# Performance work log

Hardware: AMD Instinct MI355X
Metric: run time of the kernel (lower is better)

The kernel has to match this reference:

```python
import jax, jax.numpy as jnp
import numpy as np

N = 100000      # nodes
E = 1600000     # edges
D_IN = 128
D_H = 128
D_OUT = 32
NUM_LAYERS = 3


def setup_inputs() -> dict:
    key = jax.random.key(0)
    ks = jax.random.split(key, 12)
    x = jax.random.normal(ks[0], (N, D_IN), dtype=jnp.float32)
    edge_index = jax.random.randint(ks[1], (2, E), 0, N, dtype=jnp.int64)
    def lin(k, fan_in, fan_out):
        bound = 1.0 / np.sqrt(fan_in)
        kw, kb = jax.random.split(k)
        W = jax.random.uniform(kw, (fan_in, fan_out), jnp.float32, -bound, bound)
        b = jax.random.uniform(kb, (fan_out,), jnp.float32, -bound, bound)
        return W, b
    W0, b0 = lin(ks[2], D_IN, D_H)
    W1, b1 = lin(ks[3], D_H, D_H)
    W2, b2 = lin(ks[4], D_H, D_H)
    Wfc, bfc = lin(ks[5], D_H, D_OUT)
    return {"x": x, "edge_index": edge_index, "W0": W0, "b0": b0,
            "W1": W1, "b1": b1, "W2": W2, "b2": b2, "Wfc": Wfc, "bfc": bfc}


def reference(x, edge_index, W0, b0, W1, b1, W2, b2, Wfc, bfc):
    n = x.shape[0]
    # add self-loops once (PyG GCNConv default add_self_loops=True)
    loop = jnp.arange(n, dtype=edge_index.dtype)
    src = jnp.concatenate([edge_index[0], loop])  # [E+N]
    dst = jnp.concatenate([edge_index[1], loop])
    # symmetric degree normalization: deg computed over destination (col)
    deg = jax.ops.segment_sum(jnp.ones_like(dst, dtype=x.dtype), dst, num_segments=n)
    dis = jnp.where(deg > 0, jax.lax.rsqrt(deg), 0.0)  # deg^{-1/2}, inf->0
    norm = (dis[src] * dis[dst])[:, None]              # [E+N, 1]

    def gcn_conv(h, W, b):
        h = h @ W                                       # [N, d_out]
        agg = jax.ops.segment_sum(h[src] * norm, dst, num_segments=n)
        return agg + b                                  # bias after aggregation

    h = x
    for (W, b) in ((W0, b0), (W1, b1), (W2, b2)):
        h = jax.nn.relu(gcn_conv(h, W, b))              # dropout p=0 -> identity
    pooled = jnp.mean(h, axis=0)                        # [D_H]
    return pooled @ Wfc + bfc                           # [D_OUT]
```

## Files before the change

### kernel.cpp

```cpp
#include <hip/hip_runtime.h>
#include <hip/hip_bf16.h>
#include <cstdint>


typedef unsigned short u16;
typedef unsigned int u32;
typedef unsigned char u8;
typedef __attribute__((ext_vector_type(8))) short short8v;
typedef __attribute__((ext_vector_type(4))) float f32x4;
typedef __attribute__((ext_vector_type(2))) float f32x2;

#define NBMAX 256
#define BKSH  9
#define SCH   2048
#define CAP   12288

__device__ inline u16 f2bf(float f) {
  u32 u = __float_as_uint(f);
  u += 0x7fff + ((u >> 16) & 1);
  return (u16)(u >> 16);
}
__device__ inline float bflo(u32 u) { return __uint_as_float(u << 16); }
__device__ inline float bfhi(u32 u) { return __uint_as_float(u & 0xffff0000u); }

__global__ void k_init(const int* __restrict__ ei, int* __restrict__ mode,
                       int* __restrict__ bucketCur, float* __restrict__ pooled,
                       int e, int nb) {
  if (blockIdx.x == 0) {
    __shared__ int any;
    if (threadIdx.x == 0) any = 0;
    __syncthreads();
    int lim = min(e, 2048);
    int local = 0;
    for (int i = threadIdx.x; i < lim; i += blockDim.x)
      local |= (ei[2 * i + 1] != 0);
    if (local) atomicOr(&any, 1);
    __syncthreads();
    if (threadIdx.x == 0) mode[0] = (any == 0) ? 1 : 0;
  } else {
    int i = threadIdx.x;
    if (i < nb) bucketCur[i] = 0;
    if (i < 128) pooled[i] = 0.0f;
  }
}

__global__ __launch_bounds__(256) void b_scatter(const int* __restrict__ ei,
                                                 const int* __restrict__ mode,
                                                 int* __restrict__ bucketCur,
                                                 int* __restrict__ pairBuf,
                                                 int e, int nb) {
  __shared__ int cnt[NBMAX];
  __shared__ int pre[NBMAX];
  __shared__ int base[NBMAX];
  __shared__ int stage[2 * SCH];
  const int t = threadIdx.x;
  const int chunk0 = blockIdx.x * SCH;
  const int nloc = min(SCH, e - chunk0);
  const int m = mode[0];

  cnt[t] = 0;
  __syncthreads();

  int myS[SCH / 256], myD[SCH / 256], myB[SCH / 256], mySlot[SCH / 256];
#pragma unroll
  for (int j = 0; j < SCH / 256; ++j) {
    int li = j * 256 + t;
    myB[j] = -1;
    if (li < nloc) {
      int i = chunk0 + li;
      long long di = (long long)e + i;
      int s = m ? ei[2 * (long long)i] : ei[i];
      int d = m ? ei[2 * di] : ei[di];
      int b = d >> BKSH;
      myS[j] = s; myD[j] = d; myB[j] = b;
      mySlot[j] = atomicAdd(&cnt[b], 1);
    }
  }
  __syncthreads();

  int c0 = cnt[t];
  pre[t] = c0;
  __syncthreads();
  for (int d = 1; d < NBMAX; d <<= 1) {
    int v = (t >= d) ? pre[t - d] : 0;
    __syncthreads();
    pre[t] += v;
    __syncthreads();
  }
  int myPre = pre[t] - c0;
  if (t < nb && c0 > 0) base[t] = atomicAdd(&bucketCur[t], c0);
  __syncthreads();
  cnt[t] = myPre;
  __syncthreads();

#pragma unroll
  for (int j = 0; j < SCH / 256; ++j) {
    if (myB[j] >= 0) {
      int si = cnt[myB[j]] + mySlot[j];
      stage[2 * si] = myS[j];
      stage[2 * si + 1] = myD[j];
    }
  }
  __syncthreads();

  int wave = t >> 6, lane = t & 63;
  for (int b = wave; b < nb; b += 4) {
    int cb = pre[b] - cnt[b];
    if (cb <= 0) continue;
    int lo = cnt[b];
    int gb = base[b];
    int room = CAP - gb;
    int allowed = (room > 0) ? min(cb, room) : 0;
    size_t dst = ((size_t)b * CAP + gb) * 2;
    for (int j = lane; j < 2 * allowed; j += 64)
      pairBuf[dst + j] = stage[2 * lo + j];
  }
}

__global__ __launch_bounds__(256) void b_bscan2(const int* __restrict__ bucketCur,
                                                int* __restrict__ bucketOff, int nb) {
  __shared__ int sh[NBMAX];
  int t = threadIdx.x;
  int c = (t < nb) ? bucketCur[t] : 0;
  sh[t] = c;
  __syncthreads();
  for (int d = 1; d < NBMAX; d <<= 1) {
    int v = (t >= d) ? sh[t - d] : 0;
    __syncthreads();
    sh[t] += v;
    __syncthreads();
  }
  if (t < nb) bucketOff[t] = sh[t] - c;
}

__global__ __launch_bounds__(512) void b_fine(const int* __restrict__ pairBuf,
                                              const int* __restrict__ bucketCur,
                                              const int* __restrict__ bucketOff,
                                              int* __restrict__ offs,
                                              float* __restrict__ dis,
                                              int* __restrict__ csr,
                                              int n, int e) {
  const int b = blockIdx.x;
  const int d0 = b << BKSH;
  const size_t pb = (size_t)b * CAP;
  const int cnt = bucketCur[b];
  const int lo = bucketOff[b];
  __shared__ int arr[1 << BKSH];
  __shared__ int cur[1 << BKSH];
  const int t = threadIdx.x;
  arr[t] = 0; cur[t] = 0;
  __syncthreads();
  for (int i = t; i < cnt; i += 512) {
    int d = pairBuf[2 * (pb + i) + 1];
    atomicAdd(&arr[d - d0], 1);
  }
  __syncthreads();
  int c0 = arr[t];
  __syncthreads();
  for (int dd = 1; dd < 512; dd <<= 1) {
    int v = (t >= dd) ? arr[t - dd] : 0;
    __syncthreads();
    arr[t] += v;
    __syncthreads();
  }
  int epre = arr[t] - c0;
  int gd = d0 + t;
  if (gd < n) {
    offs[gd] = lo + epre;
    dis[gd] = rsqrtf((float)c0 + 1.0f);
  }
  __syncthreads();
  arr[t] = epre;
  __syncthreads();
  for (int i = t; i < cnt; i += 512) {
    int s = pairBuf[2 * (pb + i)];
    int d = pairBuf[2 * (pb + i) + 1];
    int ld = d - d0;
    int p = lo + arr[ld] + atomicAdd(&cur[ld], 1);
    csr[p] = s;
  }
  if (b == 0 && t == 0) offs[n] = e;
}

__global__ __launch_bounds__(256) void k_wpack3(const float* __restrict__ W0,
                                                const float* __restrict__ W1,
                                                const float* __restrict__ W2,
                                                u16* __restrict__ wp) {
  int f = blockIdx.x * 256 + threadIdx.x;
  int wsel = f >> 11;
  int li = f & 2047;
  const float* W = (wsel == 0) ? W0 : (wsel == 1) ? W1 : W2;
  u16* dst = wp + (size_t)wsel * 2048 * 8;
  int ct = li >> 8, kc = (li >> 6) & 3, lane = li & 63;
  int g = lane >> 4, c = lane & 15;
  u32 o[4];
#pragma unroll
  for (int q = 0; q < 4; ++q) {
    int k = kc * 32 + g * 8 + q * 2;
    u16 e0 = f2bf(W[(size_t)k * 128 + ct * 16 + c]);
    u16 e1 = f2bf(W[(size_t)(k + 1) * 128 + ct * 16 + c]);
    o[q] = (u32)e0 | ((u32)e1 << 16);
  }
  uint4 v; v.x = o[0]; v.y = o[1]; v.z = o[2]; v.w = o[3];
  *reinterpret_cast<uint4*>(dst + (size_t)li * 8) = v;
}

template <bool FP32IN>
__global__ __launch_bounds__(256) void k_gemm_mfma(const void* __restrict__ hin,
                                                   const u16* __restrict__ wp,
                                                   const float* __restrict__ dis,
                                                   u8* __restrict__ tmpf8, int n) {
  __shared__ float eps[64 * 132];
  const int tid = threadIdx.x;
  const int w = tid >> 6, l = tid & 63;
  const int g = l >> 4, c16 = l & 15;
  const int rowbase = blockIdx.x * 64 + w * 16;

  const short8v zero8 = {0, 0, 0, 0, 0, 0, 0, 0};
  short8v a[4];
  int ar = rowbase + c16;
  bool aok = ar < n;
#pragma unroll
  for (int kc = 0; kc < 4; ++kc) {
    if (FP32IN) {
      const float* hrow = (const float*)hin + (size_t)ar * 128;
      short8v s = zero8;
      if (aok) {
        float4 v0 = *reinterpret_cast<const float4*>(hrow + kc * 32 + g * 8);
        float4 v1 = *reinterpret_cast<const float4*>(hrow + kc * 32 + g * 8 + 4);
        s[0] = (short)f2bf(v0.x); s[1] = (short)f2bf(v0.y);
        s[2] = (short)f2bf(v0.z); s[3] = (short)f2bf(v0.w);
        s[4] = (short)f2bf(v1.x); s[5] = (short)f2bf(v1.y);
        s[6] = (short)f2bf(v1.z); s[7] = (short)f2bf(v1.w);
      }
      a[kc] = s;
    } else {
      const u16* hrow = (const u16*)hin + (size_t)ar * 128;
      a[kc] = aok ? *reinterpret_cast<const short8v*>(hrow + kc * 32 + g * 8) : zero8;
    }
  }

  f32x4 acc[8];
#pragma unroll
  for (int ct = 0; ct < 8; ++ct) acc[ct] = f32x4{0.f, 0.f, 0.f, 0.f};

#pragma unroll
  for (int ct = 0; ct < 8; ++ct) {
#pragma unroll
    for (int kc = 0; kc < 4; ++kc) {
      short8v b = *reinterpret_cast<const short8v*>(wp + ((size_t)(ct * 4 + kc) * 64 + l) * 8);
      acc[ct] = __builtin_amdgcn_mfma_f32_16x16x32_bf16(a[kc], b, acc[ct], 0, 0, 0);
    }
  }

#pragma unroll
  for (int j = 0; j < 4; ++j) {
    int rl = w * 16 + g * 4 + j;
    int gr = blockIdx.x * 64 + rl;
    float dn = (gr < n) ? dis[gr] * 16.0f : 0.f;
#pragma unroll
    for (int ct = 0; ct < 8; ++ct)
      eps[rl * 132 + ct * 16 + c16] = acc[ct][j] * dn;
  }
  __syncthreads();

  int rl = tid >> 2, seg = tid & 3;
  int gr = blockIdx.x * 64 + rl;
  if (gr < n) {
    const float* src = &eps[rl * 132 + seg * 32];
    u32 wds[8];
#pragma unroll
    for (int q = 0; q < 4; ++q) {
      float4 v0 = *reinterpret_cast<const float4*>(src + q * 8);
      float4 v1 = *reinterpret_cast<const float4*>(src + q * 8 + 4);
      int p0 = __builtin_amdgcn_cvt_pk_fp8_f32(v0.x, v0.y, 0, false);
      p0 = __builtin_amdgcn_cvt_pk_fp8_f32(v0.z, v0.w, p0, true);
      int p1 = __builtin_amdgcn_cvt_pk_fp8_f32(v1.x, v1.y, 0, false);
      p1 = __builtin_amdgcn_cvt_pk_fp8_f32(v1.z, v1.w, p1, true);
      wds[q * 2] = (u32)p0;
      wds[q * 2 + 1] = (u32)p1;
    }
    uint4 o0; o0.x = wds[0]; o0.y = wds[1]; o0.z = wds[2]; o0.w = wds[3];
    uint4 o1; o1.x = wds[4]; o1.y = wds[5]; o1.z = wds[6]; o1.w = wds[7];
    *reinterpret_cast<uint4*>(tmpf8 + (size_t)gr * 128 + seg * 32) = o0;
    *reinterpret_cast<uint4*>(tmpf8 + (size_t)gr * 128 + seg * 32 + 16) = o1;
  }
}

__global__ __launch_bounds__(256) void k_gather_f8(const u8* __restrict__ tmpf8,
                                                   const int* __restrict__ csr,
                                                   const int* __restrict__ offs,
                                                   const float* __restrict__ dis,
                                                   const float* __restrict__ bias,
                                                   u16* __restrict__ houtb, int n) {
  int node0 = blockIdx.x * 8 + (threadIdx.x >> 6) * 2;
  if (node0 >= n) return;
  int node1 = node0 + 1;
  bool has1 = node1 < n;
  int lane = threadIdx.x & 63;
  const u16* tp = reinterpret_cast<const u16*>(tmpf8) + lane;

  int s0  = __builtin_amdgcn_readfirstlane(offs[node0]);
  int mid = __builtin_amdgcn_readfirstlane(offs[node1]);
  int s1  = has1 ? __builtin_amdgcn_readfirstlane(offs[node1 + 1]) : mid;

  f32x2 accA[4], accB[4];
#pragma unroll
  for (int i = 0; i < 4; ++i) { accA[i] = f32x2{0.f, 0.f}; accB[i] = f32x2{0.f, 0.f}; }

  accA[1] += __builtin_amdgcn_cvt_pk_f32_fp8((int)tp[(u32)node0 << 6], false);
  if (has1)
    accB[1] += __builtin_amdgcn_cvt_pk_f32_fp8((int)tp[(u32)node1 << 6], false);

  int e = s0;
  for (; e + 7 < s1; e += 8) {
    int ro[8];
#pragma unroll
    for (int j = 0; j < 8; ++j)
      ro[j] = __builtin_amdgcn_readfirstlane(csr[e + j]) << 6;
    u32 v[8];
#pragma unroll
    for (int j = 0; j < 8; ++j) v[j] = tp[(u32)ro[j]];
#pragma unroll
    for (int j = 0; j < 8; ++j) {
      f32x2 f = __builtin_amdgcn_cvt_pk_f32_fp8((int)v[j], false);
      if (e + j < mid) accA[j & 3] += f; else accB[j & 3] += f;
    }
  }
  for (; e < s1; ++e) {
    int r = __builtin_amdgcn_readfirstlane(csr[e]) << 6;
    f32x2 f = __builtin_amdgcn_cvt_pk_f32_fp8((int)tp[(u32)r], false);
    if (e < mid) accA[0] += f; else accB[0] += f;
  }

  float2 bb = reinterpret_cast<const float2*>(bias)[lane];
  {
    f32x2 s = (accA[0] + accA[1]) + (accA[2] + accA[3]);
    float dn = dis[node0] * 0.0625f;
    float rx = fmaf(dn, s.x, bb.x);
    float ry = fmaf(dn, s.y, bb.y);
    rx = rx > 0.f ? rx : 0.f;
    ry = ry > 0.f ? ry : 0.f;
    u32 o = (u32)f2bf(rx) | ((u32)f2bf(ry) << 16);
    reinterpret_cast<u32*>(houtb)[(size_t)node0 * 64 + lane] = o;
  }
  if (has1) {
    f32x2 s = (accB[0] + accB[1]) + (accB[2] + accB[3]);
    float dn = dis[node1] * 0.0625f;
    float rx = fmaf(dn, s.x, bb.x);
    float ry = fmaf(dn, s.y, bb.y);
    rx = rx > 0.f ? rx : 0.f;
    ry = ry > 0.f ? ry : 0.f;
    u32 o = (u32)f2bf(rx) | ((u32)f2bf(ry) << 16);
    reinterpret_cast<u32*>(houtb)[(size_t)node1 * 64 + lane] = o;
  }
}

__global__ __launch_bounds__(256) void k_pool_bf(const u16* __restrict__ h,
                                                 float* __restrict__ pooled, int n) {
  int lane = threadIdx.x & 63, wv = threadIdx.x >> 6;
  const u32* hp = reinterpret_cast<const u32*>(h);
  float sx = 0.f, sy = 0.f;
  for (int r = blockIdx.x * 4 + wv; r < n; r += gridDim.x * 4) {
    u32 u = hp[(size_t)r * 64 + lane];
    sx += bflo(u); sy += bfhi(u);
  }
  __shared__ float red[2][256];
  red[0][threadIdx.x] = sx;
  red[1][threadIdx.x] = sy;
  __syncthreads();
  if (threadIdx.x < 64) {
    float tx = red[0][threadIdx.x] + red[0][threadIdx.x + 64] +
               red[0][threadIdx.x + 128] + red[0][threadIdx.x + 192];
    float ty = red[1][threadIdx.x] + red[1][threadIdx.x + 64] +
               red[1][threadIdx.x + 128] + red[1][threadIdx.x + 192];
    atomicAdd(&pooled[threadIdx.x * 2], tx);
    atomicAdd(&pooled[threadIdx.x * 2 + 1], ty);
  }
}

__global__ void k_final(const float* __restrict__ pooled, const float* __restrict__ Wfc,
                        const float* __restrict__ bfc, float* __restrict__ out,
                        float invn) {
  int j = threadIdx.x;
  if (j < 32) {
    float acc = 0.f;
    for (int k = 0; k < 128; ++k) acc = fmaf(pooled[k], Wfc[k * 32 + j], acc);
    out[j] = fmaf(acc, invn, bfc[j]);
  }
}

extern "C" void kernel_launch(void* const* d_in, const int* in_sizes, int n_in,
                              void* d_out, int out_size, void* d_ws, size_t ws_size,
                              hipStream_t stream) {
  const float* x   = (const float*)d_in[0];
  const int*   ei  = (const int*)d_in[1];
  const float* W0  = (const float*)d_in[2];
  const float* b0  = (const float*)d_in[3];
  const float* W1  = (const float*)d_in[4];
  const float* b1  = (const float*)d_in[5];
  const float* W2  = (const float*)d_in[6];
  const float* b2  = (const float*)d_in[7];
  const float* Wfc = (const float*)d_in[8];
  const float* bfc = (const float*)d_in[9];

  const int n = in_sizes[0] / 128;
  const int e = in_sizes[1] / 2;
  const int nb = (n + (1 << BKSH) - 1) >> BKSH;

  char* ws = (char*)d_ws;
  size_t off = 0;
  auto alloc = [&](size_t bytes) -> void* {
    void* p = ws + off;
    off = (off + bytes + 255) & ~(size_t)255;
    return p;
  };
  int*   mode      = (int*)alloc(sizeof(int));
  int*   bucketCur = (int*)alloc(NBMAX * 4);
  int*   bucketOff = (int*)alloc((NBMAX + 1) * 4);
  int*   offs      = (int*)alloc((size_t)(n + 1) * 4);
  float* dis       = (float*)alloc((size_t)n * 4);
  int*   csr       = (int*)alloc((size_t)e * 4);
  float* pooled    = (float*)alloc(128 * 4);
  u16*   wp        = (u16*)alloc(3 * 2048 * 8 * 2);
  u8*    tmpf8     = (u8*)alloc((size_t)n * 128);
  u16*   houtb     = (u16*)alloc((size_t)n * 128 * 2);
  int*   pairBuf   = (int*)houtb;

  k_init<<<2, 256, 0, stream>>>(ei, mode, bucketCur, pooled, e, nb);
  b_scatter<<<(e + SCH - 1) / SCH, 256, 0, stream>>>(ei, mode, bucketCur, pairBuf, e, nb);
  b_bscan2<<<1, 256, 0, stream>>>(bucketCur, bucketOff, nb);
  b_fine<<<nb, 512, 0, stream>>>(pairBuf, bucketCur, bucketOff, offs, dis, csr, n, e);

  k_wpack3<<<24, 256, 0, stream>>>(W0, W1, W2, wp);

  int gg = (n + 63) / 64;
  int gn = (n + 7) / 8;

  k_gemm_mfma<true><<<gg, 256, 0, stream>>>(x, wp, dis, tmpf8, n);
  k_gather_f8<<<gn, 256, 0, stream>>>(tmpf8, csr, offs, dis, b0, houtb, n);
  k_gemm_mfma<false><<<gg, 256, 0, stream>>>(houtb, wp + 2048 * 8, dis, tmpf8, n);
  k_gather_f8<<<gn, 256, 0, stream>>>(tmpf8, csr, offs, dis, b1, houtb, n);
  k_gemm_mfma<false><<<gg, 256, 0, stream>>>(houtb, wp + 2 * 2048 * 8, dis, tmpf8, n);
  k_gather_f8<<<gn, 256, 0, stream>>>(tmpf8, csr, offs, dis, b2, houtb, n);

  k_pool_bf<<<512, 256, 0, stream>>>(houtb, pooled, n);
  k_final<<<1, 32, 0, stream>>>(pooled, Wfc, bfc, (float*)d_out, 1.0f / (float)n);
}
```

Baseline: 325.1 us.

## Split wavefront halves across two nodes in fp8 gather with 4-byte loads

Reworks the gather kernel so each wavefront half handles one of its two destination nodes, with each lane loading 4 fp8 values (u32) instead of 2. Both neighbor lists are walked in lockstep batches of 8, and out-of-range entries are masked with a multiply-by-zero selector. This is meant to serialize fewer edges per wavefront and use wider loads. The cost is wasted work when the two degrees are unbalanced, plus extra scalar index loads for both lists.

Measured after the change: 292.1 us. -10.1%, faster.

```diff
diff --git a/kernel.cpp b/kernel.cpp
--- a/kernel.cpp
+++ b/kernel.cpp
@@ -295,65 +295,71 @@
                                                    u16* __restrict__ houtb, int n) {
   int node0 = blockIdx.x * 8 + (threadIdx.x >> 6) * 2;
   if (node0 >= n) return;
-  int node1 = node0 + 1;
-  bool has1 = node1 < n;
+  int node1 = (node0 + 1 < n) ? node0 + 1 : node0;
   int lane = threadIdx.x & 63;
-  const u16* tp = reinterpret_cast<const u16*>(tmpf8) + lane;
+  int half = lane >> 5;
+  int l32 = lane & 31;
+  const u32* tp = reinterpret_cast<const u32*>(tmpf8) + l32;
 
   int s0  = __builtin_amdgcn_readfirstlane(offs[node0]);
   int mid = __builtin_amdgcn_readfirstlane(offs[node1]);
-  int s1  = has1 ? __builtin_amdgcn_readfirstlane(offs[node1 + 1]) : mid;
-
-  f32x2 accA[4], accB[4];
-#pragma unroll
-  for (int i = 0; i < 4; ++i) { accA[i] = f32x2{0.f, 0.f}; accB[i] = f32x2{0.f, 0.f}; }
-
-  accA[1] += __builtin_amdgcn_cvt_pk_f32_fp8((int)tp[(u32)node0 << 6], false);
-  if (has1)
-    accB[1] += __builtin_amdgcn_cvt_pk_f32_fp8((int)tp[(u32)node1 << 6], false);
-
-  int e = s0;
-  for (; e + 7 < s1; e += 8) {
+  int s1  = __builtin_amdgcn_readfirstlane(offs[node1 + 1]);
+  int len0 = mid - s0, len1 = s1 - mid;
+  int nbatch = (max(len0, len1) + 7) >> 3;
+  int midm1 = max(mid - 1, 0);
+  int s1m1  = max(s1 - 1, 0);
+
+  int myNode = half ? node1 : node0;
+
+  f32x4 acc[4];
+#pragma unroll
+  for (int i = 0; i < 4; ++i) acc[i] = f32x4{0.f, 0.f, 0.f, 0.f};
+
+  {
+    u32 v = tp[(u32)myNode << 5];
+    f32x2 lo = __builtin_amdgcn_cvt_pk_f32_fp8((int)v, false);
+    f32x2 hi = __builtin_amdgcn_cvt_pk_f32_fp8((int)v, true);
+    acc[0] += f32x4{lo.x, lo.y, hi.x, hi.y};
+  }
+
+  for (int b = 0; b < nbatch; ++b) {
+    int e0 = s0 + b * 8, e1 = mid + b * 8;
     int ro[8];
-#pragma unroll
-    for (int j = 0; j < 8; ++j)
-      ro[j] = __builtin_amdgcn_readfirstlane(csr[e + j]) << 6;
+    float sel[8];
+#pragma unroll
+    for (int j = 0; j < 8; ++j) {
+      int iA = min(e0 + j, midm1);
+      int iB = min(e1 + j, s1m1);
+      int roA = __builtin_amdgcn_readfirstlane(csr[iA]) << 5;
+      int roB = __builtin_amdgcn_readfirstlane(csr[iB]) << 5;
+      ro[j] = half ? roB : roA;
+      float sA = (e0 + j < mid) ? 1.0f : 0.0f;
+      float sB = (e1 + j < s1) ? 1.0f : 0.0f;
+      sel[j] = half ? sB : sA;
+    }
     u32 v[8];
 #pragma unroll
     for (int j = 0; j < 8; ++j) v[j] = tp[(u32)ro[j]];
 #pragma unroll
     for (int j = 0; j < 8; ++j) {
-      f32x2 f = __builtin_amdgcn_cvt_pk_f32_fp8((int)v[j], false);
-      if (e + j < mid) accA[j & 3] += f; else accB[j & 3] += f;
-    }
-  }
-  for (; e < s1; ++e) {
-    int r = __builtin_amdgcn_readfirstlane(csr[e]) << 6;
-    f32x2 f = __builtin_amdgcn_cvt_pk_f32_fp8((int)tp[(u32)r], false);
-    if (e < mid) accA[0] += f; else accB[0] += f;
-  }
-
-  float2 bb = reinterpret_cast<const float2*>(bias)[lane];
-  {
-    f32x2 s = (accA[0] + accA[1]) + (accA[2] + accA[3]);
-    float dn = dis[node0] * 0.0625f;
-    float rx = fmaf(dn, s.x, bb.x);
-    float ry = fmaf(dn, s.y, bb.y);
-    rx = rx > 0.f ? rx : 0.f;
-    ry = ry > 0.f ? ry : 0.f;
-    u32 o = (u32)f2bf(rx) | ((u32)f2bf(ry) << 16);
-    reinterpret_cast<u32*>(houtb)[(size_t)node0 * 64 + lane] = o;
-  }
-  if (has1) {
-    f32x2 s = (accB[0] + accB[1]) + (accB[2] + accB[3]);
-    float dn = dis[node1] * 0.0625f;
-    float rx = fmaf(dn, s.x, bb.x);
-    float ry = fmaf(dn, s.y, bb.y);
-    rx = rx > 0.f ? rx : 0.f;
-    ry = ry > 0.f ? ry : 0.f;
-    u32 o = (u32)f2bf(rx) | ((u32)f2bf(ry) << 16);
-    reinterpret_cast<u32*>(houtb)[(size_t)node1 * 64 + lane] = o;
-  }
+      f32x2 lo = __builtin_amdgcn_cvt_pk_f32_fp8((int)v[j], false);
+      f32x2 hi = __builtin_amdgcn_cvt_pk_f32_fp8((int)v[j], true);
+      f32x4 f = {lo.x, lo.y, hi.x, hi.y};
+      acc[j & 3] += f * sel[j];
+    }
+  }
+
+  f32x4 s = (acc[0] + acc[1]) + (acc[2] + acc[3]);
+  float dn = (half ? dis[node1] : dis[node0]) * 0.0625f;
+  float4 bb = reinterpret_cast<const float4*>(bias)[l32];
+  float r0 = fmaf(dn, s.x, bb.x); r0 = r0 > 0.f ? r0 : 0.f;
+  float r1 = fmaf(dn, s.y, bb.y); r1 = r1 > 0.f ? r1 : 0.f;
+  float r2 = fmaf(dn, s.z, bb.z); r2 = r2 > 0.f ? r2 : 0.f;
+  float r3 = fmaf(dn, s.w, bb.w); r3 = r3 > 0.f ? r3 : 0.f;
+  uint2 o;
+  o.x = (u32)f2bf(r0) | ((u32)f2bf(r1) << 16);
+  o.y = (u32)f2bf(r2) | ((u32)f2bf(r3) << 16);
+  reinterpret_cast<uint2*>(houtb)[(size_t)myNode * 32 + l32] = o;
 }
 
 __global__ __launch_bounds__(256) void k_pool_bf(const u16* __restrict__ h,
```
